# Performance work log

Hardware: AMD Instinct MI355X
Metric: run time of the kernel (lower is better)

The kernel has to match this reference:

```python
import jax, jax.numpy as jnp
import numpy as np

D_MODEL = 1024
H = 16
D_K = D_MODEL // H
D_FF = 4096
EPS = 1e-6


def layer_norm(x, alpha, bias):
    mean = jnp.mean(x, axis=-1, keepdims=True)
    var = jnp.mean((x - mean) ** 2, axis=-1, keepdims=True)  # unbiased=False
    return alpha * (x - mean) / jnp.sqrt(var + EPS) + bias


def setup_inputs() -> dict:
    key = jax.random.key(0)
    ks = jax.random.split(key, 8)
    B, S = 4, 2048
    sd = 1.0 / np.sqrt(D_MODEL)
    x = jax.random.normal(ks[0], (B, S, D_MODEL), dtype=jnp.float32)
    src_mask = jnp.ones((B, 1, S), dtype=jnp.int32)
    wq = jax.random.normal(ks[1], (D_MODEL, D_MODEL), jnp.float32) * sd
    wk = jax.random.normal(ks[2], (D_MODEL, D_MODEL), jnp.float32) * sd
    wv = jax.random.normal(ks[3], (D_MODEL, D_MODEL), jnp.float32) * sd
    wo = jax.random.normal(ks[4], (D_MODEL, D_MODEL), jnp.float32) * sd
    w1 = jax.random.normal(ks[5], (D_FF, D_MODEL), jnp.float32) * sd
    b1 = jnp.zeros((D_FF,), jnp.float32)
    w2 = jax.random.normal(ks[6], (D_MODEL, D_FF), jnp.float32) * (1.0 / np.sqrt(D_FF))
    b2 = jnp.zeros((D_MODEL,), jnp.float32)
    ln1_a = jnp.ones((D_MODEL,), jnp.float32)
    ln1_b = jnp.zeros((D_MODEL,), jnp.float32)
    ln2_a = jnp.ones((D_MODEL,), jnp.float32)
    ln2_b = jnp.zeros((D_MODEL,), jnp.float32)
    return dict(x=x, src_mask=src_mask, wq=wq, wk=wk, wv=wv, wo=wo,
                ln1_a=ln1_a, ln1_b=ln1_b, ln2_a=ln2_a, ln2_b=ln2_b,
                w1=w1, b1=b1, w2=w2, b2=b2)


def attention(xn, wq, wk, wv, wo, src_mask):
    B, S, _ = xn.shape
    # torch nn.Linear: y = x @ W.T
    q = (xn @ wq.T).reshape(B, S, H, D_K).transpose(0, 2, 1, 3)  # [B,H,S,Dk]
    k = (xn @ wk.T).reshape(B, S, H, D_K).transpose(0, 2, 1, 3)
    v = (xn @ wv.T).reshape(B, S, H, D_K).transpose(0, 2, 1, 3)
    scores = jnp.einsum('bhqd,bhkd->bhqk', q, k) / np.sqrt(D_K)
    m = src_mask[:, None, :, :]  # [B,1,1,S] from [B,1,S]
    scores = jnp.where(m == 0, -jnp.inf, scores)
    attn = jax.nn.softmax(scores, axis=-1)
    out = jnp.einsum('bhqk,bhkd->bhqd', attn, v)
    out = out.transpose(0, 2, 1, 3).reshape(B, S, D_MODEL)
    return out @ wo.T


def reference(x, src_mask, wq, wk, wv, wo, ln1_a, ln1_b, ln2_a, ln2_b, w1, b1, w2, b2):
    # pre-LN residual 1: self-attention
    xn = layer_norm(x, ln1_a, ln1_b)
    x = x + attention(xn, wq, wk, wv, wo, src_mask)
    # pre-LN residual 2: FFN
    xn = layer_norm(x, ln2_a, ln2_b)
    h = jax.nn.relu(xn @ w1.T + b1)
    x = x + (h @ w2.T + b2)
    return x
```

## Files before the change

kernel.cpp:

```cpp
#include <hip/hip_runtime.h>
#include <stdint.h>

typedef unsigned short u16;
typedef __bf16 bf16x8 __attribute__((ext_vector_type(8)));
typedef float   f32x4 __attribute__((ext_vector_type(4)));
typedef u16     u16x8 __attribute__((ext_vector_type(8)));
typedef u16     u16x4 __attribute__((ext_vector_type(4)));

__device__ __forceinline__ u16 f2bf(float f) {
    union { float f; uint32_t i; } c; c.f = f;
    uint32_t r = c.i + 0x7FFFu + ((c.i >> 16) & 1u);
    return (u16)(r >> 16);
}
__device__ __forceinline__ uint32_t cvt_pk_bf16(float lo, float hi) {
    uint32_t r;
    asm("v_cvt_pk_bf16_f32 %0, %1, %2" : "=v"(r) : "v"(lo), "v"(hi));
    return r;
}
__device__ __forceinline__ void gload_lds16(const u16* g, u16* l) {
    __builtin_amdgcn_global_load_lds(
        (__attribute__((address_space(1))) void*)(g),
        (__attribute__((address_space(3))) void*)(l), 16, 0, 0);
}
template<int N>
__device__ __forceinline__ void wait_vm_barrier() {
    asm volatile("s_waitcnt vmcnt(%0)\n\ts_barrier" :: "n"(N) : "memory");
}

__global__ __launch_bounds__(256) void cvt_all(
    const float* __restrict__ wq, const float* __restrict__ wk,
    const float* __restrict__ wv, const float* __restrict__ wo,
    const float* __restrict__ w1, const float* __restrict__ w2,
    u16* __restrict__ wqb, u16* __restrict__ wkb, u16* __restrict__ wvb,
    u16* __restrict__ wob, u16* __restrict__ w1b, u16* __restrict__ w2b)
{
    int blk = blockIdx.x;
    const float* src; u16* dst; int off;
    if      (blk < 1024)  { src = wq; dst = wqb; off = blk; }
    else if (blk < 2048)  { src = wk; dst = wkb; off = blk - 1024; }
    else if (blk < 3072)  { src = wv; dst = wvb; off = blk - 2048; }
    else if (blk < 4096)  { src = wo; dst = wob; off = blk - 3072; }
    else if (blk < 8192)  { src = w1; dst = w1b; off = blk - 4096; }
    else                  { src = w2; dst = w2b; off = blk - 8192; }
    int i = off * 1024 + threadIdx.x * 4;
    float4 v = *(const float4*)(src + i);
    u16x4 o; o[0] = f2bf(v.x); o[1] = f2bf(v.y); o[2] = f2bf(v.z); o[3] = f2bf(v.w);
    *(u16x4*)(dst + i) = o;
}

__global__ __launch_bounds__(256) void ln_kernel(
    const float* __restrict__ x, const float* __restrict__ ga,
    const float* __restrict__ be, u16* __restrict__ out)
{
    const int D = 1024;
    int row  = blockIdx.x * 4 + (threadIdx.x >> 6);
    int lane = threadIdx.x & 63;
    const float* xr = x + (size_t)row * D + lane * 16;
    float f[16];
#pragma unroll
    for (int i = 0; i < 4; ++i) *(float4*)&f[i * 4] = *(const float4*)(xr + i * 4);
    float s = 0.f, s2 = 0.f;
#pragma unroll
    for (int i = 0; i < 16; ++i) { s += f[i]; s2 += f[i] * f[i]; }
#pragma unroll
    for (int off = 1; off < 64; off <<= 1) {
        s  += __shfl_xor(s,  off, 64);
        s2 += __shfl_xor(s2, off, 64);
    }
    float mean = s * (1.0f / 1024.0f);
    float var  = s2 * (1.0f / 1024.0f) - mean * mean;
    var = var < 0.f ? 0.f : var;
    float inv = 1.0f / sqrtf(var + 1e-6f);
    float g[16], b[16];
#pragma unroll
    for (int i = 0; i < 4; ++i) {
        *(float4*)&g[i * 4] = *(const float4*)(ga + lane * 16 + i * 4);
        *(float4*)&b[i * 4] = *(const float4*)(be + lane * 16 + i * 4);
    }
    u16x8 o0, o1;
#pragma unroll
    for (int i = 0; i < 8; ++i) {
        o0[i] = f2bf(g[i]     * (f[i]     - mean) * inv + b[i]);
        o1[i] = f2bf(g[8 + i] * (f[8 + i] - mean) * inv + b[8 + i]);
    }
    u16* orow = out + (size_t)row * D + lane * 16;
    *(u16x8*)(orow)     = o0;
    *(u16x8*)(orow + 8) = o1;
}

__device__ __forceinline__ void gemm128q_core(
    const u16* __restrict__ A, const u16* __restrict__ W,
    int K, int ldw, int row_a0, int row_w0,
    u16* smem, f32x4 (&acc)[4][2])
{
    int tid  = threadIdx.x;
    int lane = tid & 63;
    int quad = lane >> 4, l16 = lane & 15;
    int wave = tid >> 6;
    int wm = wave >> 2, wn = wave & 3;

    const u16* a0 = A + (size_t)(row_a0 + (tid >> 2)) * K   + (tid & 3) * 8;
    const u16* b0 = W + (size_t)(row_w0 + (tid >> 2)) * ldw + (tid & 3) * 8;
    u16* dst = smem + tid * 8;
    const int nk = K >> 5;

#pragma unroll
    for (int s = 0; s < 3; ++s) {
        gload_lds16(a0 + s * 32, dst + s * 8192);
        gload_lds16(b0 + s * 32, dst + s * 8192 + 4096);
    }
    const int abase = (wm * 64 + l16) * 32 + quad * 8;
    const int bbase = 4096 + (wn * 32 + l16) * 32 + quad * 8;
    wait_vm_barrier<4>();

    int cb = 0, nb = 16384;
    for (int t = 0; t < nk; ++t) {
        if (t + 2 < nk) {
            gload_lds16(a0 + (t + 2) * 32, dst + nb);
            gload_lds16(b0 + (t + 2) * 32, dst + nb + 4096);
        }
        const u16* buf = smem + cb;
        bf16x8 af[4], bf[2];
#pragma unroll
        for (int mt = 0; mt < 4; ++mt)
            af[mt] = *(const bf16x8*)(&buf[abase + mt * 512]);
#pragma unroll
        for (int nt = 0; nt < 2; ++nt)
            bf[nt] = *(const bf16x8*)(&buf[bbase + nt * 512]);
#pragma unroll
        for (int mt = 0; mt < 4; ++mt)
#pragma unroll
            for (int nt = 0; nt < 2; ++nt)
                acc[mt][nt] = __builtin_amdgcn_mfma_f32_16x16x32_bf16(
                    af[mt], bf[nt], acc[mt][nt], 0, 0, 0);
        if      (t + 2 < nk) wait_vm_barrier<2>();
        else if (t + 1 < nk) wait_vm_barrier<0>();
        cb = (cb == 16384) ? 0 : cb + 8192;
        nb = (nb == 16384) ? 0 : nb + 8192;
    }
}

template<bool OUTF32>
__global__ __launch_bounds__(512, 4) void gemm128q(
    const u16* __restrict__ A, const u16* __restrict__ W,
    const float* __restrict__ bias, const float* __restrict__ resid,
    void* __restrict__ Cp, int M, int N, int K, int ldw, int do_relu)
{
    __shared__ u16 smem[24576];
    int tid  = threadIdx.x;
    int lane = tid & 63, wave = tid >> 6;
    int quad = lane >> 4, l16 = lane & 15;
    int wm = wave >> 2, wn = wave & 3;
    const int row_a0 = blockIdx.x * 128, row_w0 = blockIdx.y * 128;
    f32x4 acc[4][2] = {};
    gemm128q_core(A, W, K, ldw, row_a0, row_w0, smem, acc);
#pragma unroll
    for (int mt = 0; mt < 4; ++mt) {
#pragma unroll
        for (int nt = 0; nt < 2; ++nt) {
#pragma unroll
            for (int r = 0; r < 4; ++r) {
                int grow = row_a0 + wm * 64 + mt * 16 + quad * 4 + r;
                int gcol = row_w0 + wn * 32 + nt * 16 + l16;
                float vv = acc[mt][nt][r];
                if (bias)    vv += bias[gcol];
                if (do_relu) vv = vv > 0.f ? vv : 0.f;
                if (resid)   vv += resid[(size_t)grow * N + gcol];
                if (OUTF32) ((float*)Cp)[(size_t)grow * N + gcol] = vv;
                else        ((u16*)Cp)[(size_t)grow * N + gcol] = f2bf(vv);
            }
        }
    }
}

__global__ __launch_bounds__(512, 4) void gemm128q_qkv(
    const u16* __restrict__ A, const u16* __restrict__ Wqkv,
    u16* __restrict__ qo, u16* __restrict__ ko, u16* __restrict__ vo, int K)
{
    __shared__ u16 smem[24576];
    int tid  = threadIdx.x;
    int lane = tid & 63, wave = tid >> 6;
    int quad = lane >> 4, l16 = lane & 15;
    int wm = wave >> 2, wn = wave & 3;
    const int row_a0 = blockIdx.x * 128, row_w0 = blockIdx.y * 128;
    f32x4 acc[4][2] = {};
    gemm128q_core(A, Wqkv, K, K, row_a0, row_w0, smem, acc);
    int seg = row_w0 >> 10;
    u16* dst = (seg == 0) ? qo : (seg == 1) ? ko : vo;
    int col0 = row_w0 & 1023;
#pragma unroll
    for (int mt = 0; mt < 4; ++mt) {
#pragma unroll
        for (int nt = 0; nt < 2; ++nt) {
#pragma unroll
            for (int r = 0; r < 4; ++r) {
                int grow = row_a0 + wm * 64 + mt * 16 + quad * 4 + r;
                int gcol = col0 + wn * 32 + nt * 16 + l16;
                dst[(size_t)grow * 1024 + gcol] = f2bf(acc[mt][nt][r]);
            }
        }
    }
}

__global__ __launch_bounds__(512, 4) void attn_kernel(
    const u16* __restrict__ Q, const u16* __restrict__ Km, const u16* __restrict__ Vm,
    const int* __restrict__ mask, u16* __restrict__ O)
{
    const int S = 2048, DM = 1024;
    const float C1 = 0.18033688f;
    const float C0 = -11.541560f;
    __shared__ u16 smem[35840];
    u16* Ks0 = smem;
    u16* Ks1 = smem + 4096;
    u16* Vt0 = smem + 8192;
    u16* Vt1 = smem + 12800;
    u16* Ps  = smem + 17408;
    u16* Qs  = smem + 17408;

    int qt = blockIdx.x, bh = blockIdx.y;
    int b = bh >> 4, h = bh & 15;
    int tid = threadIdx.x;
    int wave = tid >> 6, lane = tid & 63;
    int quad = lane >> 4, l16 = lane & 15;
    size_t base = (size_t)b * S;
    size_t hoff = (size_t)h * 64;

    {
        int r = tid >> 1, c0 = (tid & 1) * 32;
        const u16* src = Q + (base + qt * 256 + r) * DM + hoff + c0;
        u16* dq = Qs + r * 72 + c0;
        *(u16x8*)(dq)      = *(const u16x8*)(src);
        *(u16x8*)(dq + 8)  = *(const u16x8*)(src + 8);
        *(u16x8*)(dq + 16) = *(const u16x8*)(src + 16);
        *(u16x8*)(dq + 24) = *(const u16x8*)(src + 24);
    }
    const u16* ksrc = Km + (base + (tid >> 3)) * DM + hoff
                    + ((tid & 7) ^ ((tid >> 5) & 7)) * 8;
    int kp = tid & 31, d0 = (tid >> 5) * 4;
    const u16* vsrc = Vm + (base + kp * 2) * DM + hoff + d0;
    const int* msrc = mask + b * S + 4 * l16;

    __syncthreads();
    const int q0 = wave * 32;
    bf16x8 qf00 = *(const bf16x8*)(&Qs[(q0 + l16) * 72 + quad * 8]);
    bf16x8 qf01 = *(const bf16x8*)(&Qs[(q0 + l16) * 72 + 32 + quad * 8]);
    bf16x8 qf10 = *(const bf16x8*)(&Qs[(q0 + 16 + l16) * 72 + quad * 8]);
    bf16x8 qf11 = *(const bf16x8*)(&Qs[(q0 + 16 + l16) * 72 + 32 + quad * 8]);
    const int swz = (l16 & 7) * 8;
    const int u0  = (quad * 8) ^ swz;

    {
        u16x4 va = *(const u16x4*)(vsrc);
        u16x4 vb = *(const u16x4*)(vsrc + DM);
        gload_lds16(ksrc, Ks0 + tid * 8);
        ksrc += 64 * DM; vsrc += 64 * DM;
#pragma unroll
        for (int i = 0; i < 4; ++i) {
            uint32_t w = (uint32_t)va[i] | ((uint32_t)vb[i] << 16);
            *(uint32_t*)(&Vt0[(d0 + i) * 72 + kp * 2]) = w;
        }
    }
    __syncthreads();

    float l0[4] = {0.f, 0.f, 0.f, 0.f};
    float l1[4] = {0.f, 0.f, 0.f, 0.f};
    f32x4 o0[4] = {}, o1[4] = {};

    for (int it = 0; it < 32; ++it) {
        const u16* Kcur = (it & 1) ? Ks1 : Ks0;
        const u16* Vcur = (it & 1) ? Vt1 : Vt0;
        u16* Knxt = (it & 1) ? Ks0 : Ks1;
        u16* Vnxt = (it & 1) ? Vt0 : Vt1;
        const bool pfch = (it < 31);
        u16x4 va, vb;
        if (pfch) {
            va = *(const u16x4*)(vsrc);
            vb = *(const u16x4*)(vsrc + DM);
            gload_lds16(ksrc, Knxt + tid * 8);
            ksrc += 64 * DM; vsrc += 64 * DM;
        }
        f32x4 s0[4] = {}, s1[4] = {};
#pragma unroll
        for (int t = 0; t < 4; ++t) {
            const u16* krp = Kcur + (4 * l16 + t) * 64;
            bf16x8 kf0 = *(const bf16x8*)(krp + u0);
            bf16x8 kf1 = *(const bf16x8*)(krp + (u0 ^ 32));
            s0[t] = __builtin_amdgcn_mfma_f32_16x16x32_bf16(qf00, kf0, s0[t], 0, 0, 0);
            s0[t] = __builtin_amdgcn_mfma_f32_16x16x32_bf16(qf01, kf1, s0[t], 0, 0, 0);
            s1[t] = __builtin_amdgcn_mfma_f32_16x16x32_bf16(qf10, kf0, s1[t], 0, 0, 0);
            s1[t] = __builtin_amdgcn_mfma_f32_16x16x32_bf16(qf11, kf1, s1[t], 0, 0, 0);
        }
        int4 mk4 = *(const int4*)(msrc); msrc += 64;
        float c0t[4];
        c0t[0] = (mk4.x == 0) ? -1e38f : C0;
        c0t[1] = (mk4.y == 0) ? -1e38f : C0;
        c0t[2] = (mk4.z == 0) ? -1e38f : C0;
        c0t[3] = (mk4.w == 0) ? -1e38f : C0;
#pragma unroll
        for (int r = 0; r < 4; ++r) {
            float p0 = exp2f(fmaf(s0[0][r], C1, c0t[0]));
            float p1 = exp2f(fmaf(s0[1][r], C1, c0t[1]));
            float p2 = exp2f(fmaf(s0[2][r], C1, c0t[2]));
            float p3 = exp2f(fmaf(s0[3][r], C1, c0t[3]));
            l0[r] += (p0 + p1) + (p2 + p3);
            uint2 pw;
            pw.x = cvt_pk_bf16(p0, p1);
            pw.y = cvt_pk_bf16(p2, p3);
            *(uint2*)(&Ps[(q0 + quad * 4 + r) * 72 + 4 * l16]) = pw;
        }
#pragma unroll
        for (int r = 0; r < 4; ++r) {
            float p0 = exp2f(fmaf(s1[0][r], C1, c0t[0]));
            float p1 = exp2f(fmaf(s1[1][r], C1, c0t[1]));
            float p2 = exp2f(fmaf(s1[2][r], C1, c0t[2]));
            float p3 = exp2f(fmaf(s1[3][r], C1, c0t[3]));
            l1[r] += (p0 + p1) + (p2 + p3);
            uint2 pw;
            pw.x = cvt_pk_bf16(p0, p1);
            pw.y = cvt_pk_bf16(p2, p3);
            *(uint2*)(&Ps[(q0 + 16 + quad * 4 + r) * 72 + 4 * l16]) = pw;
        }
        bf16x8 pf00 = *(const bf16x8*)(&Ps[(q0 + l16) * 72 + quad * 8]);
        bf16x8 pf01 = *(const bf16x8*)(&Ps[(q0 + l16) * 72 + 32 + quad * 8]);
        bf16x8 pf10 = *(const bf16x8*)(&Ps[(q0 + 16 + l16) * 72 + quad * 8]);
        bf16x8 pf11 = *(const bf16x8*)(&Ps[(q0 + 16 + l16) * 72 + 32 + quad * 8]);
#pragma unroll
        for (int t = 0; t < 4; ++t) {
            bf16x8 vf0 = *(const bf16x8*)(&Vcur[(t * 16 + l16) * 72 + quad * 8]);
            bf16x8 vf1 = *(const bf16x8*)(&Vcur[(t * 16 + l16) * 72 + 32 + quad * 8]);
            o0[t] = __builtin_amdgcn_mfma_f32_16x16x32_bf16(pf00, vf0, o0[t], 0, 0, 0);
            o0[t] = __builtin_amdgcn_mfma_f32_16x16x32_bf16(pf01, vf1, o0[t], 0, 0, 0);
            o1[t] = __builtin_amdgcn_mfma_f32_16x16x32_bf16(pf10, vf0, o1[t], 0, 0, 0);
            o1[t] = __builtin_amdgcn_mfma_f32_16x16x32_bf16(pf11, vf1, o1[t], 0, 0, 0);
        }
        if (pfch) {
#pragma unroll
            for (int i = 0; i < 4; ++i) {
                uint32_t w = (uint32_t)va[i] | ((uint32_t)vb[i] << 16);
                *(uint32_t*)(&Vnxt[(d0 + i) * 72 + kp * 2]) = w;
            }
        }
        __syncthreads();
    }
#pragma unroll
    for (int r = 0; r < 4; ++r) {
#pragma unroll
        for (int off = 1; off < 16; off <<= 1) {
            l0[r] += __shfl_xor(l0[r], off, 16);
            l1[r] += __shfl_xor(l1[r], off, 16);
        }
        float i0 = 1.0f / l0[r];
        float i1 = 1.0f / l1[r];
        u16* dst0 = O + (base + qt * 256 + q0 + quad * 4 + r) * DM + hoff + l16;
        u16* dst1 = dst0 + (size_t)16 * DM;
#pragma unroll
        for (int t = 0; t < 4; ++t) {
            dst0[t * 16] = f2bf(o0[t][r] * i0);
            dst1[t * 16] = f2bf(o1[t][r] * i1);
        }
    }
}

extern "C" void kernel_launch(void* const* d_in, const int* in_sizes, int n_in,
                              void* d_out, int out_size, void* d_ws, size_t ws_size,
                              hipStream_t stream)
{
    (void)in_sizes; (void)n_in; (void)out_size; (void)ws_size;
    const float* x    = (const float*)d_in[0];
    const int*   mask = (const int*)d_in[1];
    const float* wq   = (const float*)d_in[2];
    const float* wk   = (const float*)d_in[3];
    const float* wv   = (const float*)d_in[4];
    const float* wo   = (const float*)d_in[5];
    const float* ln1a = (const float*)d_in[6];
    const float* ln1b = (const float*)d_in[7];
    const float* ln2a = (const float*)d_in[8];
    const float* ln2b = (const float*)d_in[9];
    const float* w1   = (const float*)d_in[10];
    const float* b1   = (const float*)d_in[11];
    const float* w2   = (const float*)d_in[12];
    const float* b2   = (const float*)d_in[13];

    const int M = 8192, D = 1024, F = 4096;
    char* ws = (char*)d_ws;
    u16*  wqkv = (u16*)(ws);
    u16*  wqb = wqkv;
    u16*  wkb = (u16*)(ws + (2u  << 20));
    u16*  wvb = (u16*)(ws + (4u  << 20));
    u16*  wob = (u16*)(ws + (6u  << 20));
    u16*  w1b = (u16*)(ws + (8u  << 20));
    u16*  w2b = (u16*)(ws + (16u << 20));
    u16*  xn  = (u16*)(ws + (24u << 20));
    u16*  q   = (u16*)(ws + (40u << 20));
    u16*  hb  = (u16*)(ws + (40u << 20));

    u16*   kbuf = (u16*)d_out;
    u16*   vbuf = (u16*)d_out + (size_t)M * D;
    float* x1   = (float*)d_out;

    cvt_all<<<12288, 256, 0, stream>>>(wq, wk, wv, wo, w1, w2,
                                       wqb, wkb, wvb, wob, w1b, w2b);

    ln_kernel<<<M / 4, 256, 0, stream>>>(x, ln1a, ln1b, xn);
    dim3 gq(M / 128, 3072 / 128);
    gemm128q_qkv<<<gq, 512, 0, stream>>>(xn, wqkv, q, kbuf, vbuf, D);
    dim3 ga(2048 / 256, 64);
    attn_kernel<<<ga, 512, 0, stream>>>(q, kbuf, vbuf, mask, xn);
    dim3 g1(M / 128, D / 128);
    gemm128q<true ><<<g1, 512, 0, stream>>>(xn, wob, nullptr, x, x1, M, D, D, D, 0);
    ln_kernel<<<M / 4, 256, 0, stream>>>(x1, ln2a, ln2b, xn);
    dim3 gf1(M / 128, 2048 / 128);
    dim3 gf2(M / 128, D / 128);
    gemm128q<false><<<gf1, 512, 0, stream>>>(xn, w1b, b1, nullptr, hb, M, 2048, D, D, 1);
    gemm128q<true ><<<gf2, 512, 0, stream>>>(hb, w2b, nullptr, x1, x1, M, D, 2048, F, 0);
    gemm128q<false><<<gf1, 512, 0, stream>>>(xn, w1b + (size_t)2048 * D, b1 + 2048, nullptr, hb, M, 2048, D, D, 1);
    gemm128q<true ><<<gf2, 512, 0, stream>>>(hb, w2b + 2048, b2, x1, x1, M, D, 2048, F, 0);
}
```

Measured before the change: 561.8 us.

## Compute transposed scores and keep P in registers via permlane swaps

Attention now computes S^T (K as the A operand, Q as B), so each lane holds probabilities for one query across keys. The P tile is rearranged into the MFMA A-operand layout with permlane32/16 swaps instead of a round trip through LDS. The K swizzle and mask indexing change to match, and the row-sum reduction becomes a cross-quad shuffle. This removes the LDS writes and reads for P in each iteration, in exchange for extra cross-lane permute instructions.

New measurement: 564.5 us. Within noise of the previous version (+0.5%).

```diff
diff --git a/kernel.cpp b/kernel.cpp
--- a/kernel.cpp
+++ b/kernel.cpp
@@ -25,6 +25,28 @@
 template<int N>
 __device__ __forceinline__ void wait_vm_barrier() {
     asm volatile("s_waitcnt vmcnt(%0)\n\ts_barrier" :: "n"(N) : "memory");
+}
+__device__ __forceinline__ void pl_swap2(uint32_t &a, uint32_t &b) {
+#if defined(__has_builtin)
+#if __has_builtin(__builtin_amdgcn_permlane32_swap) && __has_builtin(__builtin_amdgcn_permlane16_swap)
+    typedef unsigned uv2 __attribute__((ext_vector_type(2)));
+    uv2 r1 = __builtin_amdgcn_permlane32_swap(a, b, false, false);
+    uv2 r2 = __builtin_amdgcn_permlane16_swap(r1[0], r1[1], false, false);
+    a = r2[0]; b = r2[1];
+    return;
+#endif
+#endif
+    int ln = threadIdx.x;
+    uint32_t as = __shfl_xor(a, 32, 64), bs = __shfl_xor(b, 32, 64);
+    uint32_t a1 = (ln & 32) ? bs : a;
+    uint32_t b1 = (ln & 32) ? b  : as;
+    as = __shfl_xor(a1, 16, 64); bs = __shfl_xor(b1, 16, 64);
+    a = (ln & 16) ? bs : a1;
+    b = (ln & 16) ? b1 : as;
+}
+__device__ __forceinline__ bf16x8 pk4(uint32_t a, uint32_t b, uint32_t c, uint32_t d) {
+    union { uint32_t u[4]; bf16x8 f; } z;
+    z.u[0] = a; z.u[1] = b; z.u[2] = c; z.u[3] = d; return z.f;
 }
 
 __global__ __launch_bounds__(256) void cvt_all(
@@ -214,7 +236,6 @@
     u16* Ks1 = smem + 4096;
     u16* Vt0 = smem + 8192;
     u16* Vt1 = smem + 12800;
-    u16* Ps  = smem + 17408;
     u16* Qs  = smem + 17408;
 
     int qt = blockIdx.x, bh = blockIdx.y;
@@ -235,10 +256,10 @@
         *(u16x8*)(dq + 24) = *(const u16x8*)(src + 24);
     }
     const u16* ksrc = Km + (base + (tid >> 3)) * DM + hoff
-                    + ((tid & 7) ^ ((tid >> 5) & 7)) * 8;
+                    + ((tid & 7) ^ ((tid >> 4) & 7)) * 8;
     int kp = tid & 31, d0 = (tid >> 5) * 4;
     const u16* vsrc = Vm + (base + kp * 2) * DM + hoff + d0;
-    const int* msrc = mask + b * S + 4 * l16;
+    const int* msrc = mask + b * S + 4 * quad;
 
     __syncthreads();
     const int q0 = wave * 32;
@@ -246,8 +267,7 @@
     bf16x8 qf01 = *(const bf16x8*)(&Qs[(q0 + l16) * 72 + 32 + quad * 8]);
     bf16x8 qf10 = *(const bf16x8*)(&Qs[(q0 + 16 + l16) * 72 + quad * 8]);
     bf16x8 qf11 = *(const bf16x8*)(&Qs[(q0 + 16 + l16) * 72 + 32 + quad * 8]);
-    const int swz = (l16 & 7) * 8;
-    const int u0  = (quad * 8) ^ swz;
+    const int kpos = (quad ^ (l16 >> 1)) * 8;
 
     {
         u16x4 va = *(const u16x4*)(vsrc);
@@ -262,8 +282,7 @@
     }
     __syncthreads();
 
-    float l0[4] = {0.f, 0.f, 0.f, 0.f};
-    float l1[4] = {0.f, 0.f, 0.f, 0.f};
+    float lacc0 = 0.f, lacc1 = 0.f;
     f32x4 o0[4] = {}, o1[4] = {};
 
     for (int it = 0; it < 32; ++it) {
@@ -279,59 +298,65 @@
             gload_lds16(ksrc, Knxt + tid * 8);
             ksrc += 64 * DM; vsrc += 64 * DM;
         }
-        f32x4 s0[4] = {}, s1[4] = {};
-#pragma unroll
-        for (int t = 0; t < 4; ++t) {
-            const u16* krp = Kcur + (4 * l16 + t) * 64;
-            bf16x8 kf0 = *(const bf16x8*)(krp + u0);
-            bf16x8 kf1 = *(const bf16x8*)(krp + (u0 ^ 32));
-            s0[t] = __builtin_amdgcn_mfma_f32_16x16x32_bf16(qf00, kf0, s0[t], 0, 0, 0);
-            s0[t] = __builtin_amdgcn_mfma_f32_16x16x32_bf16(qf01, kf1, s0[t], 0, 0, 0);
-            s1[t] = __builtin_amdgcn_mfma_f32_16x16x32_bf16(qf10, kf0, s1[t], 0, 0, 0);
-            s1[t] = __builtin_amdgcn_mfma_f32_16x16x32_bf16(qf11, kf1, s1[t], 0, 0, 0);
-        }
-        int4 mk4 = *(const int4*)(msrc); msrc += 64;
-        float c0t[4];
-        c0t[0] = (mk4.x == 0) ? -1e38f : C0;
-        c0t[1] = (mk4.y == 0) ? -1e38f : C0;
-        c0t[2] = (mk4.z == 0) ? -1e38f : C0;
-        c0t[3] = (mk4.w == 0) ? -1e38f : C0;
-#pragma unroll
-        for (int r = 0; r < 4; ++r) {
-            float p0 = exp2f(fmaf(s0[0][r], C1, c0t[0]));
-            float p1 = exp2f(fmaf(s0[1][r], C1, c0t[1]));
-            float p2 = exp2f(fmaf(s0[2][r], C1, c0t[2]));
-            float p3 = exp2f(fmaf(s0[3][r], C1, c0t[3]));
-            l0[r] += (p0 + p1) + (p2 + p3);
-            uint2 pw;
-            pw.x = cvt_pk_bf16(p0, p1);
-            pw.y = cvt_pk_bf16(p2, p3);
-            *(uint2*)(&Ps[(q0 + quad * 4 + r) * 72 + 4 * l16]) = pw;
-        }
-#pragma unroll
-        for (int r = 0; r < 4; ++r) {
-            float p0 = exp2f(fmaf(s1[0][r], C1, c0t[0]));
-            float p1 = exp2f(fmaf(s1[1][r], C1, c0t[1]));
-            float p2 = exp2f(fmaf(s1[2][r], C1, c0t[2]));
-            float p3 = exp2f(fmaf(s1[3][r], C1, c0t[3]));
-            l1[r] += (p0 + p1) + (p2 + p3);
-            uint2 pw;
-            pw.x = cvt_pk_bf16(p0, p1);
-            pw.y = cvt_pk_bf16(p2, p3);
-            *(uint2*)(&Ps[(q0 + 16 + quad * 4 + r) * 72 + 4 * l16]) = pw;
-        }
-        bf16x8 pf00 = *(const bf16x8*)(&Ps[(q0 + l16) * 72 + quad * 8]);
-        bf16x8 pf01 = *(const bf16x8*)(&Ps[(q0 + l16) * 72 + 32 + quad * 8]);
-        bf16x8 pf10 = *(const bf16x8*)(&Ps[(q0 + 16 + l16) * 72 + quad * 8]);
-        bf16x8 pf11 = *(const bf16x8*)(&Ps[(q0 + 16 + l16) * 72 + 32 + quad * 8]);
+        f32x4 st0[4] = {}, st1[4] = {};
+#pragma unroll
+        for (int t = 0; t < 4; ++t) {
+            const int ko = (16 * t + l16) * 64 + kpos;
+            bf16x8 kf0 = *(const bf16x8*)(&Kcur[ko]);
+            bf16x8 kf1 = *(const bf16x8*)(&Kcur[ko ^ 32]);
+            st0[t] = __builtin_amdgcn_mfma_f32_16x16x32_bf16(kf0, qf00, st0[t], 0, 0, 0);
+            st0[t] = __builtin_amdgcn_mfma_f32_16x16x32_bf16(kf1, qf01, st0[t], 0, 0, 0);
+            st1[t] = __builtin_amdgcn_mfma_f32_16x16x32_bf16(kf0, qf10, st1[t], 0, 0, 0);
+            st1[t] = __builtin_amdgcn_mfma_f32_16x16x32_bf16(kf1, qf11, st1[t], 0, 0, 0);
+        }
+        float c4[4][4];
+#pragma unroll
+        for (int t = 0; t < 4; ++t) {
+            int4 mk = *(const int4*)(msrc + 16 * t);
+            c4[t][0] = (mk.x == 0) ? -1e38f : C0;
+            c4[t][1] = (mk.y == 0) ? -1e38f : C0;
+            c4[t][2] = (mk.z == 0) ? -1e38f : C0;
+            c4[t][3] = (mk.w == 0) ? -1e38f : C0;
+        }
+        msrc += 64;
+        uint32_t w0_[4], v0_[4];
+#pragma unroll
+        for (int t = 0; t < 4; ++t) {
+            float p0 = exp2f(fmaf(st0[t][0], C1, c4[t][0]));
+            float p1 = exp2f(fmaf(st0[t][1], C1, c4[t][1]));
+            float p2 = exp2f(fmaf(st0[t][2], C1, c4[t][2]));
+            float p3 = exp2f(fmaf(st0[t][3], C1, c4[t][3]));
+            lacc0 += (p0 + p1) + (p2 + p3);
+            w0_[t] = cvt_pk_bf16(p0, p1);
+            v0_[t] = cvt_pk_bf16(p2, p3);
+        }
+        pl_swap2(w0_[0], w0_[1]); pl_swap2(v0_[0], v0_[1]);
+        pl_swap2(w0_[2], w0_[3]); pl_swap2(v0_[2], v0_[3]);
+        bf16x8 pA0 = pk4(w0_[0], v0_[0], w0_[1], v0_[1]);
+        bf16x8 pA1 = pk4(w0_[2], v0_[2], w0_[3], v0_[3]);
+        uint32_t w1_[4], v1_[4];
+#pragma unroll
+        for (int t = 0; t < 4; ++t) {
+            float p0 = exp2f(fmaf(st1[t][0], C1, c4[t][0]));
+            float p1 = exp2f(fmaf(st1[t][1], C1, c4[t][1]));
+            float p2 = exp2f(fmaf(st1[t][2], C1, c4[t][2]));
+            float p3 = exp2f(fmaf(st1[t][3], C1, c4[t][3]));
+            lacc1 += (p0 + p1) + (p2 + p3);
+            w1_[t] = cvt_pk_bf16(p0, p1);
+            v1_[t] = cvt_pk_bf16(p2, p3);
+        }
+        pl_swap2(w1_[0], w1_[1]); pl_swap2(v1_[0], v1_[1]);
+        pl_swap2(w1_[2], w1_[3]); pl_swap2(v1_[2], v1_[3]);
+        bf16x8 pB0 = pk4(w1_[0], v1_[0], w1_[1], v1_[1]);
+        bf16x8 pB1 = pk4(w1_[2], v1_[2], w1_[3], v1_[3]);
 #pragma unroll
         for (int t = 0; t < 4; ++t) {
             bf16x8 vf0 = *(const bf16x8*)(&Vcur[(t * 16 + l16) * 72 + quad * 8]);
             bf16x8 vf1 = *(const bf16x8*)(&Vcur[(t * 16 + l16) * 72 + 32 + quad * 8]);
-            o0[t] = __builtin_amdgcn_mfma_f32_16x16x32_bf16(pf00, vf0, o0[t], 0, 0, 0);
-            o0[t] = __builtin_amdgcn_mfma_f32_16x16x32_bf16(pf01, vf1, o0[t], 0, 0, 0);
-            o1[t] = __builtin_amdgcn_mfma_f32_16x16x32_bf16(pf10, vf0, o1[t], 0, 0, 0);
-            o1[t] = __builtin_amdgcn_mfma_f32_16x16x32_bf16(pf11, vf1, o1[t], 0, 0, 0);
+            o0[t] = __builtin_amdgcn_mfma_f32_16x16x32_bf16(pA0, vf0, o0[t], 0, 0, 0);
+            o0[t] = __builtin_amdgcn_mfma_f32_16x16x32_bf16(pA1, vf1, o0[t], 0, 0, 0);
+            o1[t] = __builtin_amdgcn_mfma_f32_16x16x32_bf16(pB0, vf0, o1[t], 0, 0, 0);
+            o1[t] = __builtin_amdgcn_mfma_f32_16x16x32_bf16(pB1, vf1, o1[t], 0, 0, 0);
         }
         if (pfch) {
 #pragma unroll
@@ -342,15 +367,12 @@
         }
         __syncthreads();
     }
+    lacc0 += __shfl_xor(lacc0, 16, 64); lacc0 += __shfl_xor(lacc0, 32, 64);
+    lacc1 += __shfl_xor(lacc1, 16, 64); lacc1 += __shfl_xor(lacc1, 32, 64);
 #pragma unroll
     for (int r = 0; r < 4; ++r) {
-#pragma unroll
-        for (int off = 1; off < 16; off <<= 1) {
-            l0[r] += __shfl_xor(l0[r], off, 16);
-            l1[r] += __shfl_xor(l1[r], off, 16);
-        }
-        float i0 = 1.0f / l0[r];
-        float i1 = 1.0f / l1[r];
+        float i0 = 1.0f / __shfl(lacc0, quad * 4 + r, 16);
+        float i1 = 1.0f / __shfl(lacc1, quad * 4 + r, 16);
         u16* dst0 = O + (base + qt * 256 + q0 + quad * 4 + r) * DM + hoff + l16;
         u16* dst1 = dst0 + (size_t)16 * DM;
 #pragma unroll
```
